# Optimization experiments

Hardware: AMD Instinct MI355X
Metric: run time of the kernel (lower is better)

Reference implementation:

```python
import jax, jax.numpy as jnp
import numpy as np

DIM = 1024
HEADS = 16
HEAD_DIM = DIM // HEADS  # 64
WIN = 256
B, N = 4, 4096


def setup_inputs() -> dict:
    key = jax.random.key(0)
    k1, k2, k3 = jax.random.split(key, 3)
    x = jax.random.normal(k1, (B, N, DIM), dtype=jnp.float32)
    # torch nn.Linear weights: [out_features, in_features]
    Wqkv = jax.random.normal(k2, (3 * DIM, DIM), dtype=jnp.float32) * (DIM ** -0.5)
    Wproj = jax.random.normal(k3, (DIM, DIM), dtype=jnp.float32) * (DIM ** -0.5)
    return {"x": x, "Wqkv": Wqkv, "Wproj": Wproj}


def reference(x, Wqkv, Wproj):
    Bs, Ns, C = x.shape
    H, hd, W = HEADS, HEAD_DIM, WIN
    # qkv projection -> [3, B, H, N, hd]
    qkv = (x @ Wqkv.T).reshape(Bs, Ns, 3, H, hd).transpose(2, 0, 3, 1, 4)
    q, k, v = qkv[0], qkv[1], qkv[2]
    q = q * (hd ** -0.5)
    pad = (W - Ns % W) % W
    if pad:
        pw = ((0, 0), (0, 0), (0, pad), (0, 0))
        q = jnp.pad(q, pw)
        k = jnp.pad(k, pw)
        v = jnp.pad(v, pw)
    Np = Ns + pad
    Df = (Np * hd) // W  # flattened feature dim per window row
    q = q.reshape(Bs * H, W, Df)
    k = k.reshape(Bs * H, W, Df)
    v = v.reshape(Bs * H, W, Df)
    attn = jax.nn.softmax(jnp.einsum('bwd,bxd->bwx', q, k), axis=-1)  # [B*H, W, W]
    out = jnp.einsum('bwx,bxd->bwd', attn, v)
    out = out.reshape(Bs, H, Np, hd)[:, :, :Ns, :].transpose(0, 2, 1, 3).reshape(Bs, Ns, C)
    return out @ Wproj.T
```

## Files before the change

### kernel.cpp

```cpp
#include <hip/hip_runtime.h>
#include <hip/hip_bf16.h>
#include <stdint.h>


using u16 = unsigned short;
typedef __attribute__((ext_vector_type(4))) float f32x4;
typedef __attribute__((ext_vector_type(8))) short s16x8;

#define MFMA_BF16(a, b, c) __builtin_amdgcn_mfma_f32_16x16x32_bf16((a), (b), (c), 0, 0, 0)

__device__ __forceinline__ u16 f2bf(float f) {
  union { float f; uint32_t u; } v; v.f = f;
  uint32_t r = v.u + 0x7fffu + ((v.u >> 16) & 1u);
  return (u16)(r >> 16);
}

__device__ __forceinline__ void gld16(const void* g, void* l) {
  auto gp = (const __attribute__((address_space(1))) void*)(uintptr_t)g;
  auto lp = (__attribute__((address_space(3))) void*)(uint32_t)(uintptr_t)l;
  __builtin_amdgcn_global_load_lds(gp, lp, 16, 0, 0);
}

__global__ __launch_bounds__(256) void cvt_bf16(const float* __restrict__ in,
                                                u16* __restrict__ out, int n8) {
  for (int i = blockIdx.x * blockDim.x + threadIdx.x; i < n8;
       i += gridDim.x * blockDim.x) {
    const float4* p = (const float4*)in + (size_t)i * 2;
    float4 a = p[0], b = p[1];
    s16x8 r;
    r[0] = (short)f2bf(a.x); r[1] = (short)f2bf(a.y);
    r[2] = (short)f2bf(a.z); r[3] = (short)f2bf(a.w);
    r[4] = (short)f2bf(b.x); r[5] = (short)f2bf(b.y);
    r[6] = (short)f2bf(b.z); r[7] = (short)f2bf(b.w);
    *(s16x8*)(out + (size_t)i * 8) = r;
  }
}

template <bool QS, bool F32OUT, int GN>
__global__ __launch_bounds__(512, 2) void gemm256(const u16* __restrict__ A,
                                                  const u16* __restrict__ W,
                                                  void* __restrict__ C) {
  __shared__ alignas(16) u16 lds[4 * 16384];
  const int tid = threadIdx.x;
  const int wv = tid >> 6, lane = tid & 63;
  const int fr = lane & 15, fg = lane >> 4;
  const int wm = wv >> 2, wn = wv & 3;
  const int N = GN * 256;

  const int nwg = 64 * GN;
  const int p = blockIdx.x;
  const int logical = (p & 7) * (nwg >> 3) + (p >> 3);
  const int bm = logical / GN, bn = logical % GN;

  const int srow = tid >> 2;
  const int skg = (tid & 3) ^ ((tid >> 3) & 3);

  const u16* As = A + (size_t)(bm * 256 + srow) * 1024 + skg * 8;
  const u16* Ws = W + (size_t)(bn * 256 + srow) * 1024 + skg * 8;

  const f32x4 fz = {0.f, 0.f, 0.f, 0.f};
  f32x4 acc[8][4];
#pragma unroll
  for (int i = 0; i < 8; ++i)
#pragma unroll
    for (int j = 0; j < 4; ++j) acc[i][j] = fz;

  auto STAGE_A = [&](int t) {
    u16* dst = lds + (t & 3) * 16384;
    const int k0 = t * 32;
    gld16(As + k0,          dst + wv * 512);
    gld16(As + 131072 + k0, dst + 4096 + wv * 512);
  };
  auto STAGE_B = [&](int t) {
    u16* dst = lds + (t & 3) * 16384;
    const int k0 = t * 32;
    gld16(Ws + k0,          dst + 8192 + wv * 512);
    gld16(Ws + 131072 + k0, dst + 12288 + wv * 512);
  };

  STAGE_A(0); STAGE_B(0);
  STAGE_A(1); STAGE_B(1);
  STAGE_A(2); STAGE_B(2);
  asm volatile("s_waitcnt vmcnt(8)" ::: "memory");
  __builtin_amdgcn_s_barrier();

  const int rsw = (fg ^ ((fr >> 1) & 3)) * 8;
  const int aoff = (wm * 128 + fr) * 32 + rsw;
  const int boff = 8192 + (wn * 64 + fr) * 32 + rsw;

  for (int t = 0; t < 32; ++t) {
    const u16* buf = lds + (t & 3) * 16384;
    s16x8 a0[4], a1[4], bv[4];

#pragma unroll
    for (int mi = 0; mi < 4; ++mi)
      a0[mi] = *(const s16x8*)(buf + aoff + mi * 512);
#pragma unroll
    for (int ni = 0; ni < 4; ++ni)
      bv[ni] = *(const s16x8*)(buf + boff + ni * 512);
    __builtin_amdgcn_sched_barrier(0);
#pragma unroll
    for (int mi = 0; mi < 4; ++mi)
      a1[mi] = *(const s16x8*)(buf + aoff + (4 + mi) * 512);

    if (t <= 28) {
      STAGE_A(t + 3);
      asm volatile("s_waitcnt vmcnt(6)" ::: "memory");
    } else if (t == 29) {
      asm volatile("s_waitcnt vmcnt(4)" ::: "memory");
    } else {
      asm volatile("s_waitcnt vmcnt(0)" ::: "memory");
    }
    __builtin_amdgcn_s_barrier();

    asm volatile("s_waitcnt lgkmcnt(4)" ::: "memory");
    __builtin_amdgcn_sched_barrier(0);
    __builtin_amdgcn_s_setprio(1);
#pragma unroll
    for (int ni = 0; ni < 4; ++ni)
#pragma unroll
      for (int mi = 0; mi < 4; ++mi)
        acc[mi][ni] = MFMA_BF16(a0[mi], bv[ni], acc[mi][ni]);
    __builtin_amdgcn_s_setprio(0);

    if (t <= 28) STAGE_B(t + 3);
    asm volatile("s_waitcnt lgkmcnt(0)" ::: "memory");
    __builtin_amdgcn_sched_barrier(0);
    __builtin_amdgcn_s_barrier();

    __builtin_amdgcn_s_setprio(1);
#pragma unroll
    for (int ni = 0; ni < 4; ++ni)
#pragma unroll
      for (int mi = 0; mi < 4; ++mi)
        acc[4 + mi][ni] = MFMA_BF16(a1[mi], bv[ni], acc[4 + mi][ni]);
    __builtin_amdgcn_s_setprio(0);
  }

  const float scale = (QS && bn < 4) ? 0.125f : 1.0f;
#pragma unroll
  for (int mi = 0; mi < 8; ++mi)
#pragma unroll
    for (int ni = 0; ni < 4; ++ni) {
      const int row = bm * 256 + wm * 128 + mi * 16 + fg * 4;
      const int col = bn * 256 + wn * 64 + ni * 16 + fr;
      if (F32OUT) {
        float* cp = (float*)C + (size_t)row * N + col;
#pragma unroll
        for (int r = 0; r < 4; ++r) cp[(size_t)r * N] = acc[mi][ni][r] * scale;
      } else {
        u16* cp = (u16*)C + (size_t)row * N + col;
#pragma unroll
        for (int r = 0; r < 4; ++r) cp[(size_t)r * N] = f2bf(acc[mi][ni][r] * scale);
      }
    }
}

__global__ __launch_bounds__(256) void attn_win(const u16* __restrict__ qkv,
                                                u16* __restrict__ attn) {
  const int bid = blockIdx.x;
  const int bh = (bid & 7) + ((bid >> 5) << 3);
  const int qb = (bid >> 3) & 3;
  const int b = bh >> 4, h = bh & 15;

  const int tid = threadIdx.x;
  const int wv = tid >> 6, lane = tid & 63;
  const int fr = lane & 15, fg = lane >> 4;
  const int li = lane >> 2, lc = lane & 3;

  __shared__ alignas(16) char smem[33792 + 20480];
  u16* lP = (u16*)smem;
  u16* lQ = (u16*)(smem + 33792);
  u16* lK = (u16*)(smem + 33792 + 4096);
  float* redm = (float*)(smem + 33792);
  float* reds = (float*)(smem + 33792 + 1024);
  u16* lVt = (u16*)(smem + 33792);

  const size_t qbase = (size_t)b * 4096 * 3072;

  const f32x4 fz = {0.f, 0.f, 0.f, 0.f};
  f32x4 acc[4][4];
#pragma unroll
  for (int i = 0; i < 4; ++i)
#pragma unroll
    for (int j = 0; j < 4; ++j) acc[i][j] = fz;

  for (int kt = 0; kt < 32; ++kt) {
    const size_t dofs = (size_t)(kt >> 1) * 3072 + h * 64 + (kt & 1) * 32 + lc * 8;
    {
      const int r = wv * 16 + li;
      gld16(qkv + qbase + (size_t)((qb * 64 + r) * 16) * 3072 + dofs, lQ + wv * 512);
    }
#pragma unroll
    for (int j = 0; j < 4; ++j) {
      const int q = wv * 4 + j;
      const int r = q * 16 + li;
      gld16(qkv + qbase + (size_t)(r * 16) * 3072 + 1024 + dofs, lK + q * 512);
    }
    __syncthreads();
    s16x8 qa[4];
#pragma unroll
    for (int mi = 0; mi < 4; ++mi)
      qa[mi] = *(const s16x8*)(lQ + (mi * 16 + fr) * 32 + fg * 8);
#pragma unroll
    for (int ni = 0; ni < 4; ++ni) {
      s16x8 kb = *(const s16x8*)(lK + (wv * 64 + ni * 16 + fr) * 32 + fg * 8);
#pragma unroll
      for (int mi = 0; mi < 4; ++mi)
        acc[mi][ni] = MFMA_BF16(qa[mi], kb, acc[mi][ni]);
    }
    __syncthreads();
  }

  float rmax[4][4], rnrm[4][4];
#pragma unroll
  for (int mi = 0; mi < 4; ++mi)
#pragma unroll
    for (int r = 0; r < 4; ++r) {
      float m = fmaxf(fmaxf(acc[mi][0][r], acc[mi][1][r]),
                      fmaxf(acc[mi][2][r], acc[mi][3][r]));
      for (int o = 1; o < 16; o <<= 1) m = fmaxf(m, __shfl_xor(m, o));
      rmax[mi][r] = m;
    }
  if (fr == 0) {
#pragma unroll
    for (int mi = 0; mi < 4; ++mi)
#pragma unroll
      for (int r = 0; r < 4; ++r) redm[wv * 64 + mi * 16 + fg * 4 + r] = rmax[mi][r];
  }
  __syncthreads();
#pragma unroll
  for (int mi = 0; mi < 4; ++mi)
#pragma unroll
    for (int r = 0; r < 4; ++r) {
      const int row = mi * 16 + fg * 4 + r;
      rmax[mi][r] = fmaxf(fmaxf(redm[row], redm[64 + row]),
                          fmaxf(redm[128 + row], redm[192 + row]));
    }
#pragma unroll
  for (int mi = 0; mi < 4; ++mi)
#pragma unroll
    for (int r = 0; r < 4; ++r) {
      float s = 0.f;
#pragma unroll
      for (int ni = 0; ni < 4; ++ni) {
        float p = exp2f((acc[mi][ni][r] - rmax[mi][r]) * 1.4426950408889634f);
        acc[mi][ni][r] = p;
        s += p;
      }
      for (int o = 1; o < 16; o <<= 1) s += __shfl_xor(s, o);
      rnrm[mi][r] = s;
    }
  if (fr == 0) {
#pragma unroll
    for (int mi = 0; mi < 4; ++mi)
#pragma unroll
      for (int r = 0; r < 4; ++r) reds[wv * 64 + mi * 16 + fg * 4 + r] = rnrm[mi][r];
  }
  __syncthreads();
#pragma unroll
  for (int mi = 0; mi < 4; ++mi)
#pragma unroll
    for (int r = 0; r < 4; ++r) {
      const int row = mi * 16 + fg * 4 + r;
      rnrm[mi][r] = 1.f / (reds[row] + reds[64 + row] + reds[128 + row] + reds[192 + row]);
    }
#pragma unroll
  for (int mi = 0; mi < 4; ++mi)
#pragma unroll
    for (int ni = 0; ni < 4; ++ni)
#pragma unroll
      for (int r = 0; r < 4; ++r)
        lP[(mi * 16 + fg * 4 + r) * 264 + wv * 64 + ni * 16 + fr] =
            f2bf(acc[mi][ni][r] * rnrm[mi][r]);
  __syncthreads();

#pragma unroll 1
  for (int nc = 0; nc < 4; ++nc) {
    f32x4 oacc[4][4];
#pragma unroll
    for (int i = 0; i < 4; ++i)
#pragma unroll
      for (int j = 0; j < 4; ++j) oacc[i][j] = fz;
#pragma unroll 1
    for (int xt = 0; xt < 8; ++xt) {
#pragma unroll
      for (int it = 0; it < 4; ++it) {
        const int id = it * 256 + tid;
        const int xl = id & 31, ng = id >> 5;
        const int d = nc * 256 + ng * 8;
        const u16* g = qkv + qbase +
                       (size_t)((xt * 32 + xl) * 16 + (d >> 6)) * 3072 + 2048 +
                       h * 64 + (d & 63);
        s16x8 v = *(const s16x8*)g;
#pragma unroll
        for (int i = 0; i < 8; ++i) lVt[(ng * 8 + i) * 40 + xl] = (u16)v[i];
      }
      __syncthreads();
      s16x8 pa[4];
#pragma unroll
      for (int mi = 0; mi < 4; ++mi)
        pa[mi] = *(const s16x8*)(lP + (mi * 16 + fr) * 264 + xt * 32 + fg * 8);
#pragma unroll
      for (int ni = 0; ni < 4; ++ni) {
        s16x8 vb = *(const s16x8*)(lVt + (wv * 64 + ni * 16 + fr) * 40 + fg * 8);
#pragma unroll
        for (int mi = 0; mi < 4; ++mi)
          oacc[mi][ni] = MFMA_BF16(pa[mi], vb, oacc[mi][ni]);
      }
      __syncthreads();
    }
#pragma unroll
    for (int mi = 0; mi < 4; ++mi)
#pragma unroll
      for (int ni = 0; ni < 4; ++ni) {
        const int row = mi * 16 + fg * 4;
        const int d = nc * 256 + wv * 64 + ni * 16 + fr;
        const int p = d >> 6, e = d & 63;
        const size_t base =
            (size_t)(b * 4096 + (qb * 64 + row) * 16 + p) * 1024 + h * 64 + e;
#pragma unroll
        for (int r = 0; r < 4; ++r)
          attn[base + (size_t)r * 16 * 1024] = f2bf(oacc[mi][ni][r]);
      }
  }
}

extern "C" void kernel_launch(void* const* d_in, const int* in_sizes, int n_in,
                              void* d_out, int out_size, void* d_ws, size_t ws_size,
                              hipStream_t stream) {
  (void)in_sizes; (void)n_in; (void)out_size; (void)ws_size;
  const float* x = (const float*)d_in[0];
  const float* wqkv = (const float*)d_in[1];
  const float* wproj = (const float*)d_in[2];
  float* out = (float*)d_out;

  char* ws = (char*)d_ws;
  u16* qkv = (u16*)ws;
  u16* xbf = (u16*)(ws + 100663296);
  u16* attn = xbf;
  u16* wqkvb = (u16*)(ws + 134217728);
  u16* wprojb = (u16*)(ws + 140509184);

  cvt_bf16<<<2048, 256, 0, stream>>>(x, xbf, 16777216 / 8);
  cvt_bf16<<<1536, 256, 0, stream>>>(wqkv, wqkvb, 3145728 / 8);
  cvt_bf16<<<512, 256, 0, stream>>>(wproj, wprojb, 1048576 / 8);

  gemm256<true, false, 12><<<768, 512, 0, stream>>>(xbf, wqkvb, qkv);
  attn_win<<<256, 256, 0, stream>>>(qkv, attn);
  gemm256<false, true, 4><<<256, 512, 0, stream>>>(attn, wprojb, out);
}
```

Before: 239.6 us.

## Double-buffer attention loads, widen to 8 waves, and fuse bf16 conversions

The windowed attention kernel moves from 4 to 8 waves per block, each wave owning half as many key columns. Q/K tiles are now double-buffered in LDS with an XOR swizzle, and the V transpose is software-pipelined through register prefetch into alternating LDS buffers. MFMA sections are raised in priority. The three fp32-to-bf16 conversion launches are merged into one kernel. The changes aim to hide global load latency and cut launch overhead, at the cost of more LDS (which lowers occupancy) and extra scalar V gathers.

```diff
diff --git a/kernel.cpp b/kernel.cpp
--- a/kernel.cpp
+++ b/kernel.cpp
@@ -21,18 +21,26 @@
   __builtin_amdgcn_global_load_lds(gp, lp, 16, 0, 0);
 }
 
-__global__ __launch_bounds__(256) void cvt_bf16(const float* __restrict__ in,
-                                                u16* __restrict__ out, int n8) {
-  for (int i = blockIdx.x * blockDim.x + threadIdx.x; i < n8;
-       i += gridDim.x * blockDim.x) {
-    const float4* p = (const float4*)in + (size_t)i * 2;
+__global__ __launch_bounds__(256) void cvt3(const float* __restrict__ x,
+                                            const float* __restrict__ w1,
+                                            const float* __restrict__ w2,
+                                            u16* __restrict__ ox,
+                                            u16* __restrict__ ow1,
+                                            u16* __restrict__ ow2) {
+  const int stride = gridDim.x * blockDim.x;
+  for (int i = blockIdx.x * blockDim.x + threadIdx.x; i < 2621440; i += stride) {
+    const float* src; u16* dst; int j;
+    if (i < 2097152)      { src = x;  dst = ox;  j = i; }
+    else if (i < 2490368) { src = w1; dst = ow1; j = i - 2097152; }
+    else                  { src = w2; dst = ow2; j = i - 2490368; }
+    const float4* p = (const float4*)src + (size_t)j * 2;
     float4 a = p[0], b = p[1];
     s16x8 r;
     r[0] = (short)f2bf(a.x); r[1] = (short)f2bf(a.y);
     r[2] = (short)f2bf(a.z); r[3] = (short)f2bf(a.w);
     r[4] = (short)f2bf(b.x); r[5] = (short)f2bf(b.y);
     r[6] = (short)f2bf(b.z); r[7] = (short)f2bf(b.w);
-    *(s16x8*)(out + (size_t)i * 8) = r;
+    *(s16x8*)(dst + (size_t)j * 8) = r;
   }
 }
 
@@ -156,7 +164,7 @@
     }
 }
 
-__global__ __launch_bounds__(256) void attn_win(const u16* __restrict__ qkv,
+__global__ __launch_bounds__(512) void attn_win(const u16* __restrict__ qkv,
                                                 u16* __restrict__ attn) {
   const int bid = blockIdx.x;
   const int bh = (bid & 7) + ((bid >> 5) << 3);
@@ -166,59 +174,79 @@
   const int tid = threadIdx.x;
   const int wv = tid >> 6, lane = tid & 63;
   const int fr = lane & 15, fg = lane >> 4;
-  const int li = lane >> 2, lc = lane & 3;
-
-  __shared__ alignas(16) char smem[33792 + 20480];
+
+  __shared__ alignas(16) char smem[74752];
   u16* lP = (u16*)smem;
-  u16* lQ = (u16*)(smem + 33792);
-  u16* lK = (u16*)(smem + 33792 + 4096);
-  float* redm = (float*)(smem + 33792);
-  float* reds = (float*)(smem + 33792 + 1024);
-  u16* lVt = (u16*)(smem + 33792);
+  const int SB = 33792;
+  float* redm = (float*)(smem + SB);
+  float* reds = (float*)(smem + SB + 2048);
 
   const size_t qbase = (size_t)b * 4096 * 3072;
+  const int sg = (lane & 3) ^ ((lane >> 3) & 3);
+
+  const int krow = tid >> 2;
+  const u16* Ksrc = qkv + qbase + (size_t)(krow * 16) * 3072 + 1024 + h * 64 + sg * 8;
+  const int qrow = (wv & 3) * 16 + (lane >> 2);
+  const u16* Qsrc = qkv + qbase + (size_t)((qb * 64 + qrow) * 16) * 3072 + h * 64 + sg * 8;
+
+  auto STAGE_QK = [&](int t) {
+    u16* qd = (u16*)(smem + SB + (t & 1) * 4096);
+    u16* kd = (u16*)(smem + SB + 8192 + (t & 1) * 16384);
+    const int dofs = (t >> 1) * 3072 + (t & 1) * 32;
+    gld16(Ksrc + dofs, kd + wv * 512);
+    gld16(Ksrc + (size_t)128 * 16 * 3072 + dofs, kd + 4096 + wv * 512);
+    if (wv < 4) gld16(Qsrc + dofs, qd + wv * 512);
+  };
 
   const f32x4 fz = {0.f, 0.f, 0.f, 0.f};
-  f32x4 acc[4][4];
+  f32x4 acc[4][2];
 #pragma unroll
   for (int i = 0; i < 4; ++i)
 #pragma unroll
-    for (int j = 0; j < 4; ++j) acc[i][j] = fz;
+    for (int j = 0; j < 2; ++j) acc[i][j] = fz;
+
+  const int rsw = (fg ^ ((fr >> 1) & 3)) * 8;
+
+  STAGE_QK(0);
+  asm volatile("s_waitcnt vmcnt(0)" ::: "memory");
+  __builtin_amdgcn_s_barrier();
 
   for (int kt = 0; kt < 32; ++kt) {
-    const size_t dofs = (size_t)(kt >> 1) * 3072 + h * 64 + (kt & 1) * 32 + lc * 8;
-    {
-      const int r = wv * 16 + li;
-      gld16(qkv + qbase + (size_t)((qb * 64 + r) * 16) * 3072 + dofs, lQ + wv * 512);
-    }
-#pragma unroll
-    for (int j = 0; j < 4; ++j) {
-      const int q = wv * 4 + j;
-      const int r = q * 16 + li;
-      gld16(qkv + qbase + (size_t)(r * 16) * 3072 + 1024 + dofs, lK + q * 512);
-    }
-    __syncthreads();
-    s16x8 qa[4];
-#pragma unroll
-    for (int mi = 0; mi < 4; ++mi)
-      qa[mi] = *(const s16x8*)(lQ + (mi * 16 + fr) * 32 + fg * 8);
-#pragma unroll
-    for (int ni = 0; ni < 4; ++ni) {
-      s16x8 kb = *(const s16x8*)(lK + (wv * 64 + ni * 16 + fr) * 32 + fg * 8);
+    const u16* qbuf = (const u16*)(smem + SB + (kt & 1) * 4096);
+    const u16* kbuf = (const u16*)(smem + SB + 8192 + (kt & 1) * 16384);
+    if (kt < 31) STAGE_QK(kt + 1);
+
+    s16x8 qa[4], kb[2];
+#pragma unroll
+    for (int mi = 0; mi < 4; ++mi)
+      qa[mi] = *(const s16x8*)(qbuf + (mi * 16 + fr) * 32 + rsw);
+#pragma unroll
+    for (int ni = 0; ni < 2; ++ni)
+      kb[ni] = *(const s16x8*)(kbuf + (wv * 32 + ni * 16 + fr) * 32 + rsw);
+
+    asm volatile("s_waitcnt lgkmcnt(0)" ::: "memory");
+    __builtin_amdgcn_sched_barrier(0);
+    __builtin_amdgcn_s_setprio(1);
+#pragma unroll
+    for (int ni = 0; ni < 2; ++ni)
 #pragma unroll
       for (int mi = 0; mi < 4; ++mi)
-        acc[mi][ni] = MFMA_BF16(qa[mi], kb, acc[mi][ni]);
-    }
-    __syncthreads();
-  }
+        acc[mi][ni] = MFMA_BF16(qa[mi], kb[ni], acc[mi][ni]);
+    __builtin_amdgcn_s_setprio(0);
+
+    if (kt < 31) {
+      asm volatile("s_waitcnt vmcnt(0)" ::: "memory");
+      __builtin_amdgcn_s_barrier();
+    }
+  }
+  __syncthreads();
 
   float rmax[4][4], rnrm[4][4];
 #pragma unroll
   for (int mi = 0; mi < 4; ++mi)
 #pragma unroll
     for (int r = 0; r < 4; ++r) {
-      float m = fmaxf(fmaxf(acc[mi][0][r], acc[mi][1][r]),
-                      fmaxf(acc[mi][2][r], acc[mi][3][r]));
+      float m = fmaxf(acc[mi][0][r], acc[mi][1][r]);
       for (int o = 1; o < 16; o <<= 1) m = fmaxf(m, __shfl_xor(m, o));
       rmax[mi][r] = m;
     }
@@ -234,8 +262,10 @@
 #pragma unroll
     for (int r = 0; r < 4; ++r) {
       const int row = mi * 16 + fg * 4 + r;
-      rmax[mi][r] = fmaxf(fmaxf(redm[row], redm[64 + row]),
-                          fmaxf(redm[128 + row], redm[192 + row]));
+      float m = redm[row];
+#pragma unroll
+      for (int w = 1; w < 8; ++w) m = fmaxf(m, redm[w * 64 + row]);
+      rmax[mi][r] = m;
     }
 #pragma unroll
   for (int mi = 0; mi < 4; ++mi)
@@ -243,7 +273,7 @@
     for (int r = 0; r < 4; ++r) {
       float s = 0.f;
 #pragma unroll
-      for (int ni = 0; ni < 4; ++ni) {
+      for (int ni = 0; ni < 2; ++ni) {
         float p = exp2f((acc[mi][ni][r] - rmax[mi][r]) * 1.4426950408889634f);
         acc[mi][ni][r] = p;
         s += p;
@@ -251,6 +281,7 @@
       for (int o = 1; o < 16; o <<= 1) s += __shfl_xor(s, o);
       rnrm[mi][r] = s;
     }
+  __syncthreads();
   if (fr == 0) {
 #pragma unroll
     for (int mi = 0; mi < 4; ++mi)
@@ -263,62 +294,99 @@
 #pragma unroll
     for (int r = 0; r < 4; ++r) {
       const int row = mi * 16 + fg * 4 + r;
-      rnrm[mi][r] = 1.f / (reds[row] + reds[64 + row] + reds[128 + row] + reds[192 + row]);
+      float s = reds[row];
+#pragma unroll
+      for (int w = 1; w < 8; ++w) s += reds[w * 64 + row];
+      rnrm[mi][r] = 1.f / s;
     }
 #pragma unroll
   for (int mi = 0; mi < 4; ++mi)
 #pragma unroll
-    for (int ni = 0; ni < 4; ++ni)
+    for (int ni = 0; ni < 2; ++ni)
 #pragma unroll
       for (int r = 0; r < 4; ++r)
-        lP[(mi * 16 + fg * 4 + r) * 264 + wv * 64 + ni * 16 + fr] =
+        lP[(mi * 16 + fg * 4 + r) * 264 + wv * 32 + ni * 16 + fr] =
             f2bf(acc[mi][ni][r] * rnrm[mi][r]);
   __syncthreads();
 
-#pragma unroll 1
+  u16* lVt0 = (u16*)(smem + SB);
+  u16* lVt1 = (u16*)(smem + SB + 20480);
+  const int ld = tid & 255;
+  const int jb = tid >> 8;
+
   for (int nc = 0; nc < 4; ++nc) {
-    f32x4 oacc[4][4];
+    const int d = nc * 256 + ld;
+    const u16* Vcol = qkv + qbase + (size_t)(d >> 6) * 3072 + 2048 + h * 64 + (d & 63);
+
+    f32x4 oacc[4][2];
 #pragma unroll
     for (int i = 0; i < 4; ++i)
 #pragma unroll
-      for (int j = 0; j < 4; ++j) oacc[i][j] = fz;
+      for (int j = 0; j < 2; ++j) oacc[i][j] = fz;
+
+    u16 va[2][8];
+    auto VLOAD = [&](int xt) {
+#pragma unroll
+      for (int jj = 0; jj < 2; ++jj) {
+        const int xo = (jb + 2 * jj) * 8;
+        const u16* g = Vcol + (size_t)((xt * 32 + xo) * 16) * 3072;
+#pragma unroll
+        for (int i = 0; i < 8; ++i) va[jj][i] = g[(size_t)i * 16 * 3072];
+      }
+    };
+    auto VWRITE = [&](u16* buf) {
+#pragma unroll
+      for (int jj = 0; jj < 2; ++jj) {
+        const int xo = (jb + 2 * jj) * 8;
+        s16x8 v;
+#pragma unroll
+        for (int i = 0; i < 8; ++i) v[i] = (short)va[jj][i];
+        *(s16x8*)(buf + ld * 40 + xo) = v;
+      }
+    };
+
+    VLOAD(0);
+    VWRITE(lVt0);
+
 #pragma unroll 1
     for (int xt = 0; xt < 8; ++xt) {
-#pragma unroll
-      for (int it = 0; it < 4; ++it) {
-        const int id = it * 256 + tid;
-        const int xl = id & 31, ng = id >> 5;
-        const int d = nc * 256 + ng * 8;
-        const u16* g = qkv + qbase +
-                       (size_t)((xt * 32 + xl) * 16 + (d >> 6)) * 3072 + 2048 +
-                       h * 64 + (d & 63);
-        s16x8 v = *(const s16x8*)g;
-#pragma unroll
-        for (int i = 0; i < 8; ++i) lVt[(ng * 8 + i) * 40 + xl] = (u16)v[i];
-      }
+      u16* cur = (xt & 1) ? lVt1 : lVt0;
+      u16* nxt = (xt & 1) ? lVt0 : lVt1;
       __syncthreads();
-      s16x8 pa[4];
+
+      if (xt < 7) VLOAD(xt + 1);
+
+      s16x8 pa[4], vb[2];
 #pragma unroll
       for (int mi = 0; mi < 4; ++mi)
         pa[mi] = *(const s16x8*)(lP + (mi * 16 + fr) * 264 + xt * 32 + fg * 8);
 #pragma unroll
-      for (int ni = 0; ni < 4; ++ni) {
-        s16x8 vb = *(const s16x8*)(lVt + (wv * 64 + ni * 16 + fr) * 40 + fg * 8);
+      for (int ni = 0; ni < 2; ++ni)
+        vb[ni] = *(const s16x8*)(cur + (wv * 32 + ni * 16 + fr) * 40 + fg * 8);
+
+      asm volatile("s_waitcnt lgkmcnt(0)" ::: "memory");
+      __builtin_amdgcn_sched_barrier(0);
+      __builtin_amdgcn_s_setprio(1);
+#pragma unroll
+      for (int ni = 0; ni < 2; ++ni)
 #pragma unroll
         for (int mi = 0; mi < 4; ++mi)
-          oacc[mi][ni] = MFMA_BF16(pa[mi], vb, oacc[mi][ni]);
-      }
-      __syncthreads();
-    }
-#pragma unroll
-    for (int mi = 0; mi < 4; ++mi)
-#pragma unroll
-      for (int ni = 0; ni < 4; ++ni) {
+          oacc[mi][ni] = MFMA_BF16(pa[mi], vb[ni], oacc[mi][ni]);
+      __builtin_amdgcn_s_setprio(0);
+
+      if (xt < 7) VWRITE(nxt);
+    }
+    __syncthreads();
+
+#pragma unroll
+    for (int mi = 0; mi < 4; ++mi)
+#pragma unroll
+      for (int ni = 0; ni < 2; ++ni) {
         const int row = mi * 16 + fg * 4;
-        const int d = nc * 256 + wv * 64 + ni * 16 + fr;
-        const int p = d >> 6, e = d & 63;
+        const int dd = nc * 256 + wv * 32 + ni * 16 + fr;
+        const int pp = dd >> 6, e = dd & 63;
         const size_t base =
-            (size_t)(b * 4096 + (qb * 64 + row) * 16 + p) * 1024 + h * 64 + e;
+            (size_t)(b * 4096 + (qb * 64 + row) * 16 + pp) * 1024 + h * 64 + e;
 #pragma unroll
         for (int r = 0; r < 4; ++r)
           attn[base + (size_t)r * 16 * 1024] = f2bf(oacc[mi][ni][r]);
@@ -342,11 +410,8 @@
   u16* wqkvb = (u16*)(ws + 134217728);
   u16* wprojb = (u16*)(ws + 140509184);
 
-  cvt_bf16<<<2048, 256, 0, stream>>>(x, xbf, 16777216 / 8);
-  cvt_bf16<<<1536, 256, 0, stream>>>(wqkv, wqkvb, 3145728 / 8);
-  cvt_bf16<<<512, 256, 0, stream>>>(wproj, wprojb, 1048576 / 8);
-
+  cvt3<<<2048, 256, 0, stream>>>(x, wqkv, wproj, xbf, wqkvb, wprojb);
   gemm256<true, false, 12><<<768, 512, 0, stream>>>(xbf, wqkvb, qkv);
-  attn_win<<<256, 256, 0, stream>>>(qkv, attn);
+  attn_win<<<256, 512, 0, stream>>>(qkv, attn);
   gemm256<false, true, 4><<<256, 512, 0, stream>>>(attn, wprojb, out);
 }
```

New measurement: 219.2 us. 1.09x faster.
